# Performance work log

Measured on AMD Instinct MI355X. Metric: run time of the kernel, lower is better.

Reference implementation:

```python
import jax, jax.numpy as jnp
import numpy as np


def setup_inputs() -> dict:
    key = jax.random.key(0)
    ks = jax.random.split(key, 7)
    d_in, d_out, batch = 4096, 4096, 8192
    x = jax.random.normal(ks[0], (batch, d_in), dtype=jnp.float32)
    w_loc = jax.random.normal(ks[1], (d_in, d_out), dtype=jnp.float32) * (1.0 / np.sqrt(d_in))
    w_std = jnp.full((d_in, d_out), -6.0, dtype=jnp.float32) + 0.1 * jax.random.normal(ks[2], (d_in, d_out), dtype=jnp.float32)
    b_loc = jax.random.normal(ks[3], (1, d_out), dtype=jnp.float32) * 0.02
    b_std = jnp.full((1, d_out), -6.0, dtype=jnp.float32) + 0.1 * jax.random.normal(ks[4], (1, d_out), dtype=jnp.float32)
    eps_w = jax.random.normal(ks[5], (d_in, d_out), dtype=jnp.float32)
    eps_b = jax.random.normal(ks[6], (1, d_out), dtype=jnp.float32)
    return {"x": x, "w_loc": w_loc, "w_std": w_std, "b_loc": b_loc, "b_std": b_std, "eps_w": eps_w, "eps_b": eps_b}


def reference(x, w_loc, w_std, b_loc, b_std, eps_w, eps_b):
    # Reparameterized sample: W ~ Normal(w_loc, softplus(w_std))
    w = w_loc + jax.nn.softplus(w_std) * eps_w          # [d_in, d_out]
    b = b_loc + jax.nn.softplus(b_std) * eps_b          # [1, d_out]
    return x @ w + b                                    # [batch, d_out]
```

## Files before the change

### kernel.cpp

```cpp
#include <hip/hip_runtime.h>

typedef unsigned short u16;
typedef unsigned int u32;
typedef __bf16 bf16;
typedef __attribute__((ext_vector_type(8))) bf16 bf16x8;
typedef __attribute__((ext_vector_type(4))) float f32x4;
typedef __attribute__((ext_vector_type(8))) u16 u16x8;

#define M_DIM 8192
#define N_DIM 4096
#define K_DIM 4096
#define NTK   (K_DIM / 64)

__device__ __forceinline__ u16 f2bf(float f) {
    u32 u = __float_as_uint(f);
    u32 r = (u + 0x7fffu + ((u >> 16) & 1u)) >> 16;
    return (u16)r;
}

__device__ __forceinline__ float softplus_f(float x) {
    return fmaxf(x, 0.f) + log1pf(expf(-fabsf(x)));
}

__device__ __forceinline__ void gload_lds16(const void* g, void* l) {
    __builtin_amdgcn_global_load_lds(
        (const __attribute__((address_space(1))) void*)g,
        (__attribute__((address_space(3))) void*)l,
        16, 0, 0);
}

__global__ void conv_x_kernel(const float* __restrict__ x, u16* __restrict__ xb,
                              long long n8) {
    long long idx = blockIdx.x * (long long)blockDim.x + threadIdx.x;
    long long stride = gridDim.x * (long long)blockDim.x;
    for (long long i = idx; i < n8; i += stride) {
        const float4* xp = (const float4*)(x + i * 8);
        float4 a = xp[0], b = xp[1];
        u16x8 r;
        r[0] = f2bf(a.x); r[1] = f2bf(a.y); r[2] = f2bf(a.z); r[3] = f2bf(a.w);
        r[4] = f2bf(b.x); r[5] = f2bf(b.y); r[6] = f2bf(b.z); r[7] = f2bf(b.w);
        *(u16x8*)(xb + i * 8) = r;
    }
}

__global__ void wconv_kernel(const float* __restrict__ w_loc,
                             const float* __restrict__ w_std,
                             const float* __restrict__ eps_w,
                             u16* __restrict__ wt) {
    __shared__ u16 t[64][66];
    const int kb = blockIdx.x & 63;
    const int nb = blockIdx.x >> 6;
    const int k0 = kb * 64, n0 = nb * 64;
    const int tx = threadIdx.x & 63;
    const int ty = threadIdx.x >> 6;
#pragma unroll
    for (int r = 0; r < 64; r += 4) {
        const size_t off = (size_t)(k0 + r + ty) * N_DIM + n0 + tx;
        float v = w_loc[off] + softplus_f(w_std[off]) * eps_w[off];
        t[r + ty][tx] = f2bf(v);
    }
    __syncthreads();
#pragma unroll
    for (int r = 0; r < 64; r += 4) {
        wt[(size_t)(n0 + r + ty) * K_DIM + k0 + tx] = t[tx][r + ty];
    }
}

__global__ void bias_kernel(const float* __restrict__ b_loc,
                            const float* __restrict__ b_std,
                            const float* __restrict__ eps_b,
                            float* __restrict__ bias) {
    int i = blockIdx.x * blockDim.x + threadIdx.x;
    if (i < N_DIM) bias[i] = b_loc[i] + softplus_f(b_std[i]) * eps_b[i];
}

#define MFMA_Q(O, AV, BV)                                                    \
    _Pragma("unroll") for (int i_ = 0; i_ < 4; ++i_)                         \
    _Pragma("unroll") for (int n_ = 0; n_ < 4; ++n_)                         \
        acc[(O) + i_][n_] = __builtin_amdgcn_mfma_f32_16x16x32_bf16(         \
            AV[i_], BV[n_], acc[(O) + i_][n_], 0, 0, 0);

#define PH_SYNC_IN()                                                         \
    __builtin_amdgcn_s_barrier();                                            \
    asm volatile("s_waitcnt lgkmcnt(0)" ::: "memory");                       \
    __builtin_amdgcn_sched_barrier(0);                                       \
    __builtin_amdgcn_s_setprio(1);

#define PH_SYNC_OUT()                                                        \
    __builtin_amdgcn_s_setprio(0);                                           \
    __builtin_amdgcn_s_barrier();

__global__ __launch_bounds__(512, 2) void gemm_kernel(
    const u16* __restrict__ Xb, const u16* __restrict__ Wt,
    const float* __restrict__ bias, float* __restrict__ C) {
    extern __shared__ u16 lds[];

    const int tid = threadIdx.x;
    const int l  = tid & 63;
    const int w  = tid >> 6;
    const int wm = w >> 2;
    const int wn = w & 3;

    const int swz = (blockIdx.x & 7) * 64 + (blockIdx.x >> 3);
    const int m0 = (swz >> 4) * 256;
    const int n0 = (swz & 15) * 256;

    const u16* Ab = Xb + (size_t)m0 * K_DIM;
    const u16* Bb = Wt + (size_t)n0 * K_DIM;

    const int srow = tid >> 3;
    const int sq   = ((tid & 7) ^ (srow & 7)) * 8;

    const int fr = l & 15, hi = l >> 4;
    const int cg0 = (hi ^ (fr & 7)) * 8;
    const int cg1 = cg0 ^ 32;

    auto stageA = [&](int u) {
#pragma unroll
        for (int s = 0; s < 4; ++s) {
            const u16* g = Ab + (size_t)(s * 64 + srow) * K_DIM + u * 64 + sq;
            gload_lds16(g, &lds[(u & 1) * 16384 + s * 4096 + tid * 8]);
        }
    };
    auto stageB = [&](int u) {
#pragma unroll
        for (int s = 0; s < 4; ++s) {
            const u16* g = Bb + (size_t)(s * 64 + srow) * K_DIM + u * 64 + sq;
            gload_lds16(g, &lds[32768 + (u & 1) * 16384 + s * 4096 + tid * 8]);
        }
    };

    f32x4 acc[8][4] = {};

    stageA(0); stageB(0); stageB(1);
    asm volatile("s_waitcnt vmcnt(4)" ::: "memory");
    __builtin_amdgcn_sched_barrier(0);
    __builtin_amdgcn_s_barrier();

    for (int u = 0; u < NTK; ++u) {
        const int bo = (u & 1) * 16384;
        const int bB = 32768 + bo;
        const int arow = bo + (wm * 128 + fr) * 64;
        const int brow = bB + (wn * 64 + fr) * 64;
        bf16x8 a[4], b0[4], b1[4];

#pragma unroll
        for (int n = 0; n < 4; ++n) {
            b0[n] = *(const bf16x8*)&lds[brow + n * 1024 + cg0];
            b1[n] = *(const bf16x8*)&lds[brow + n * 1024 + cg1];
        }
#pragma unroll
        for (int m = 0; m < 4; ++m)
            a[m] = *(const bf16x8*)&lds[arow + m * 1024 + cg0];
        if (u + 1 < NTK) stageA(u + 1);
        PH_SYNC_IN();
        MFMA_Q(0, a, b0);
        PH_SYNC_OUT();

#pragma unroll
        for (int m = 0; m < 4; ++m)
            a[m] = *(const bf16x8*)&lds[arow + (m + 4) * 1024 + cg0];
        if (u + 2 < NTK) stageB(u + 2);
        PH_SYNC_IN();
        MFMA_Q(4, a, b0);
        PH_SYNC_OUT();

#pragma unroll
        for (int m = 0; m < 4; ++m)
            a[m] = *(const bf16x8*)&lds[arow + m * 1024 + cg1];
        PH_SYNC_IN();
        MFMA_Q(0, a, b1);
        PH_SYNC_OUT();

#pragma unroll
        for (int m = 0; m < 4; ++m)
            a[m] = *(const bf16x8*)&lds[arow + (m + 4) * 1024 + cg1];
        __builtin_amdgcn_s_barrier();
        asm volatile("s_waitcnt lgkmcnt(0)" ::: "memory");
        __builtin_amdgcn_sched_barrier(0);
        __builtin_amdgcn_s_setprio(1);
        MFMA_Q(4, a, b1);
        __builtin_amdgcn_s_setprio(0);
        if (u + 2 < NTK) {
            asm volatile("s_waitcnt vmcnt(4)" ::: "memory");
        } else if (u + 1 < NTK) {
            asm volatile("s_waitcnt vmcnt(0)" ::: "memory");
        }
        __builtin_amdgcn_sched_barrier(0);
        __builtin_amdgcn_s_barrier();
    }

    const int orow0 = m0 + wm * 128;
    const int ocol0 = n0 + wn * 64;
    float bv[4];
#pragma unroll
    for (int n = 0; n < 4; ++n) bv[n] = bias[ocol0 + n * 16 + fr];
#pragma unroll
    for (int m = 0; m < 8; ++m)
#pragma unroll
        for (int n = 0; n < 4; ++n)
#pragma unroll
            for (int j = 0; j < 4; ++j)
                C[(size_t)(orow0 + m * 16 + hi * 4 + j) * N_DIM
                  + ocol0 + n * 16 + fr] = acc[m][n][j] + bv[n];
}

extern "C" void kernel_launch(void* const* d_in, const int* in_sizes, int n_in,
                              void* d_out, int out_size, void* d_ws, size_t ws_size,
                              hipStream_t stream) {
    const float* x     = (const float*)d_in[0];
    const float* w_loc = (const float*)d_in[1];
    const float* w_std = (const float*)d_in[2];
    const float* b_loc = (const float*)d_in[3];
    const float* b_std = (const float*)d_in[4];
    const float* eps_w = (const float*)d_in[5];
    const float* eps_b = (const float*)d_in[6];
    float* out = (float*)d_out;

    char* ws = (char*)d_ws;
    u16* Xb   = (u16*)ws;
    u16* Wt   = (u16*)(ws + (size_t)M_DIM * K_DIM * 2);
    float* bv = (float*)(ws + (size_t)M_DIM * K_DIM * 2
                            + (size_t)N_DIM * K_DIM * 2);

    (void)hipFuncSetAttribute((const void*)gemm_kernel,
                              hipFuncAttributeMaxDynamicSharedMemorySize, 131072);

    conv_x_kernel<<<2048, 256, 0, stream>>>(x, Xb, (long long)M_DIM * K_DIM / 8);
    wconv_kernel<<<(K_DIM / 64) * (N_DIM / 64), 256, 0, stream>>>(w_loc, w_std, eps_w, Wt);
    bias_kernel<<<N_DIM / 256, 256, 0, stream>>>(b_loc, b_std, eps_b, bv);
    gemm_kernel<<<(M_DIM / 256) * (N_DIM / 256), 512, 131072, stream>>>(Xb, Wt, bv, out);
}
```

Measured before the change: 354.6 us.

## Switch GEMM inner loop to 32x32x16 bf16 MFMA with four k-phases

Replaces the 16x16x32 MFMA tiling (8x4 accumulator tiles per wave) with 32x32x16 MFMA (4x2 tiles of 16 floats). This halves the number of MFMA issues and cuts the LDS fragment reads per flop. The k-loop is regrouped into four phases, and staging of the next A/B tiles is split into half-tile chunks spread across those phases. The epilogue is rewritten for the 32x32 output layout, which risks different LDS bank behaviour with the existing swizzle and more register pressure from holding all B fragments.

```diff
diff --git a/kernel.cpp b/kernel.cpp
--- a/kernel.cpp
+++ b/kernel.cpp
@@ -4,7 +4,7 @@
 typedef unsigned int u32;
 typedef __bf16 bf16;
 typedef __attribute__((ext_vector_type(8))) bf16 bf16x8;
-typedef __attribute__((ext_vector_type(4))) float f32x4;
+typedef __attribute__((ext_vector_type(16))) float f32x16;
 typedef __attribute__((ext_vector_type(8))) u16 u16x8;
 
 #define M_DIM 8192
@@ -74,22 +74,6 @@
     if (i < N_DIM) bias[i] = b_loc[i] + softplus_f(b_std[i]) * eps_b[i];
 }
 
-#define MFMA_Q(O, AV, BV)                                                    \
-    _Pragma("unroll") for (int i_ = 0; i_ < 4; ++i_)                         \
-    _Pragma("unroll") for (int n_ = 0; n_ < 4; ++n_)                         \
-        acc[(O) + i_][n_] = __builtin_amdgcn_mfma_f32_16x16x32_bf16(         \
-            AV[i_], BV[n_], acc[(O) + i_][n_], 0, 0, 0);
-
-#define PH_SYNC_IN()                                                         \
-    __builtin_amdgcn_s_barrier();                                            \
-    asm volatile("s_waitcnt lgkmcnt(0)" ::: "memory");                       \
-    __builtin_amdgcn_sched_barrier(0);                                       \
-    __builtin_amdgcn_s_setprio(1);
-
-#define PH_SYNC_OUT()                                                        \
-    __builtin_amdgcn_s_setprio(0);                                           \
-    __builtin_amdgcn_s_barrier();
-
 __global__ __launch_bounds__(512, 2) void gemm_kernel(
     const u16* __restrict__ Xb, const u16* __restrict__ Wt,
     const float* __restrict__ bias, float* __restrict__ C) {
@@ -111,98 +95,104 @@
     const int srow = tid >> 3;
     const int sq   = ((tid & 7) ^ (srow & 7)) * 8;
 
-    const int fr = l & 15, hi = l >> 4;
-    const int cg0 = (hi ^ (fr & 7)) * 8;
-    const int cg1 = cg0 ^ 32;
-
-    auto stageA = [&](int u) {
-#pragma unroll
-        for (int s = 0; s < 4; ++s) {
-            const u16* g = Ab + (size_t)(s * 64 + srow) * K_DIM + u * 64 + sq;
-            gload_lds16(g, &lds[(u & 1) * 16384 + s * 4096 + tid * 8]);
+    const int lane31 = l & 31;
+    const int hi2    = l >> 5;
+    const int rsw    = l & 7;
+
+    auto stageA = [&](int u, int h) {
+#pragma unroll
+        for (int s = 0; s < 2; ++s) {
+            const u16* g = Ab + (size_t)(h * 128 + s * 64 + srow) * K_DIM + u * 64 + sq;
+            gload_lds16(g, &lds[(u & 1) * 16384 + h * 8192 + s * 4096 + tid * 8]);
         }
     };
-    auto stageB = [&](int u) {
-#pragma unroll
-        for (int s = 0; s < 4; ++s) {
-            const u16* g = Bb + (size_t)(s * 64 + srow) * K_DIM + u * 64 + sq;
-            gload_lds16(g, &lds[32768 + (u & 1) * 16384 + s * 4096 + tid * 8]);
+    auto stageB = [&](int u, int h) {
+#pragma unroll
+        for (int s = 0; s < 2; ++s) {
+            const u16* g = Bb + (size_t)(h * 128 + s * 64 + srow) * K_DIM + u * 64 + sq;
+            gload_lds16(g, &lds[32768 + (u & 1) * 16384 + h * 8192 + s * 4096 + tid * 8]);
         }
     };
 
-    f32x4 acc[8][4] = {};
-
-    stageA(0); stageB(0); stageB(1);
+    f32x16 acc[4][2] = {};
+
+    stageA(0, 0); stageA(0, 1); stageB(0, 0); stageB(0, 1);
+    stageB(1, 0); stageB(1, 1);
     asm volatile("s_waitcnt vmcnt(4)" ::: "memory");
     __builtin_amdgcn_sched_barrier(0);
     __builtin_amdgcn_s_barrier();
 
+#define CE(KS) ((((KS) * 2 + hi2) ^ rsw) << 3)
+
+#define PHASE(KS, STAGE_STMT, DRAIN_STMT)                                     \
+        {                                                                     \
+            if ((KS) > 0) {                                                   \
+                _Pragma("unroll")                                             \
+                for (int mb = 0; mb < 4; ++mb)                                \
+                    a[mb] = *(const bf16x8*)&lds[abase + mb * 2048 + CE(KS)]; \
+            }                                                                 \
+            STAGE_STMT;                                                       \
+            __builtin_amdgcn_s_barrier();                                     \
+            asm volatile("s_waitcnt lgkmcnt(0)" ::: "memory");                \
+            __builtin_amdgcn_sched_barrier(0);                                \
+            __builtin_amdgcn_s_setprio(1);                                    \
+            _Pragma("unroll")                                                 \
+            for (int mb = 0; mb < 4; ++mb) {                                  \
+                acc[mb][0] = __builtin_amdgcn_mfma_f32_32x32x16_bf16(         \
+                    a[mb], b[KS][0], acc[mb][0], 0, 0, 0);                    \
+                acc[mb][1] = __builtin_amdgcn_mfma_f32_32x32x16_bf16(         \
+                    a[mb], b[KS][1], acc[mb][1], 0, 0, 0);                    \
+            }                                                                 \
+            __builtin_amdgcn_s_setprio(0);                                    \
+            DRAIN_STMT;                                                       \
+            __builtin_amdgcn_sched_barrier(0);                                \
+            __builtin_amdgcn_s_barrier();                                     \
+        }
+
     for (int u = 0; u < NTK; ++u) {
-        const int bo = (u & 1) * 16384;
-        const int bB = 32768 + bo;
-        const int arow = bo + (wm * 128 + fr) * 64;
-        const int brow = bB + (wn * 64 + fr) * 64;
-        bf16x8 a[4], b0[4], b1[4];
-
-#pragma unroll
-        for (int n = 0; n < 4; ++n) {
-            b0[n] = *(const bf16x8*)&lds[brow + n * 1024 + cg0];
-            b1[n] = *(const bf16x8*)&lds[brow + n * 1024 + cg1];
-        }
-#pragma unroll
-        for (int m = 0; m < 4; ++m)
-            a[m] = *(const bf16x8*)&lds[arow + m * 1024 + cg0];
-        if (u + 1 < NTK) stageA(u + 1);
-        PH_SYNC_IN();
-        MFMA_Q(0, a, b0);
-        PH_SYNC_OUT();
-
-#pragma unroll
-        for (int m = 0; m < 4; ++m)
-            a[m] = *(const bf16x8*)&lds[arow + (m + 4) * 1024 + cg0];
-        if (u + 2 < NTK) stageB(u + 2);
-        PH_SYNC_IN();
-        MFMA_Q(4, a, b0);
-        PH_SYNC_OUT();
-
-#pragma unroll
-        for (int m = 0; m < 4; ++m)
-            a[m] = *(const bf16x8*)&lds[arow + m * 1024 + cg1];
-        PH_SYNC_IN();
-        MFMA_Q(0, a, b1);
-        PH_SYNC_OUT();
-
-#pragma unroll
-        for (int m = 0; m < 4; ++m)
-            a[m] = *(const bf16x8*)&lds[arow + (m + 4) * 1024 + cg1];
-        __builtin_amdgcn_s_barrier();
-        asm volatile("s_waitcnt lgkmcnt(0)" ::: "memory");
-        __builtin_amdgcn_sched_barrier(0);
-        __builtin_amdgcn_s_setprio(1);
-        MFMA_Q(4, a, b1);
-        __builtin_amdgcn_s_setprio(0);
-        if (u + 2 < NTK) {
-            asm volatile("s_waitcnt vmcnt(4)" ::: "memory");
-        } else if (u + 1 < NTK) {
-            asm volatile("s_waitcnt vmcnt(0)" ::: "memory");
-        }
-        __builtin_amdgcn_sched_barrier(0);
-        __builtin_amdgcn_s_barrier();
-    }
+        const int abase = (u & 1) * 16384 + (wm * 128 + lane31) * 64;
+        const int bbase = 32768 + (u & 1) * 16384 + (wn * 64 + lane31) * 64;
+
+        bf16x8 a[4], b[4][2];
+#pragma unroll
+        for (int ks = 0; ks < 4; ++ks) {
+            b[ks][0] = *(const bf16x8*)&lds[bbase + CE(ks)];
+            b[ks][1] = *(const bf16x8*)&lds[bbase + 2048 + CE(ks)];
+        }
+#pragma unroll
+        for (int mb = 0; mb < 4; ++mb)
+            a[mb] = *(const bf16x8*)&lds[abase + mb * 2048 + CE(0)];
+
+        PHASE(0, { if (u + 1 < NTK) stageA(u + 1, 0); }, {});
+        PHASE(1, { if (u + 1 < NTK) stageA(u + 1, 1); }, {});
+        PHASE(2, { if (u + 2 < NTK) stageB(u + 2, 0); }, {});
+        PHASE(3, { if (u + 2 < NTK) stageB(u + 2, 1); },
+              {
+                  if (u + 2 < NTK) {
+                      asm volatile("s_waitcnt vmcnt(4)" ::: "memory");
+                  } else if (u + 1 < NTK) {
+                      asm volatile("s_waitcnt vmcnt(0)" ::: "memory");
+                  }
+              });
+    }
+#undef PHASE
+#undef CE
 
     const int orow0 = m0 + wm * 128;
     const int ocol0 = n0 + wn * 64;
-    float bv[4];
-#pragma unroll
-    for (int n = 0; n < 4; ++n) bv[n] = bias[ocol0 + n * 16 + fr];
-#pragma unroll
-    for (int m = 0; m < 8; ++m)
-#pragma unroll
-        for (int n = 0; n < 4; ++n)
-#pragma unroll
-            for (int j = 0; j < 4; ++j)
-                C[(size_t)(orow0 + m * 16 + hi * 4 + j) * N_DIM
-                  + ocol0 + n * 16 + fr] = acc[m][n][j] + bv[n];
+    float bv[2];
+    bv[0] = bias[ocol0 + lane31];
+    bv[1] = bias[ocol0 + 32 + lane31];
+#pragma unroll
+    for (int mb = 0; mb < 4; ++mb)
+#pragma unroll
+        for (int nb = 0; nb < 2; ++nb)
+#pragma unroll
+            for (int r = 0; r < 16; ++r) {
+                const int row = orow0 + mb * 32 + (r & 3) + 8 * (r >> 2) + 4 * hi2;
+                const int col = ocol0 + nb * 32 + lane31;
+                C[(size_t)row * N_DIM + col] = acc[mb][nb][r] + bv[nb];
+            }
 }
 
 extern "C" void kernel_launch(void* const* d_in, const int* in_sizes, int n_in,
```

Result: slower. 364.2 us (+2.7%).
